# Kernel tuning notes

Measured on AMD Instinct MI355X. Metric: run time of the kernel, lower is better.

The kernel has to match this reference:

```python
import jax, jax.numpy as jnp
import numpy as np

B, S, D, H, HD, F, R = 16, 512, 1024, 16, 64, 4096, 16


def setup_inputs() -> dict:
    key = jax.random.key(0)
    ks = jax.random.split(key, 24)
    sc = 0.02  # keep activations in a sane range through the deep stack
    d = {
        "x": jax.random.normal(ks[0], (B, S, D), jnp.float32),
        "w_q": jax.random.normal(ks[1], (D, D), jnp.float32) * sc,
        "b_q": jnp.zeros((D,), jnp.float32),
        "w_q_lora_a": jax.random.normal(ks[2], (D, R), jnp.float32) * sc,
        "w_q_lora_b": jax.random.normal(ks[3], (R, D), jnp.float32) * sc,
        "w_k": jax.random.normal(ks[4], (D, D), jnp.float32) * sc,
        "b_k": jnp.zeros((D,), jnp.float32),
        "w_k_lora_a": jax.random.normal(ks[5], (D, R), jnp.float32) * sc,
        "w_k_lora_b": jax.random.normal(ks[6], (R, D), jnp.float32) * sc,
        "w_v": jax.random.normal(ks[7], (D, D), jnp.float32) * sc,
        "b_v": jnp.zeros((D,), jnp.float32),
        "w_v_lora_a": jax.random.normal(ks[8], (D, R), jnp.float32) * sc,
        "w_v_lora_b": jax.random.normal(ks[9], (R, D), jnp.float32) * sc,
        "w_o": jax.random.normal(ks[10], (D, D), jnp.float32) * sc,
        "b_o": jnp.zeros((D,), jnp.float32),
        "w_o_lora_a": jax.random.normal(ks[11], (D, R), jnp.float32) * sc,
        "w_o_lora_b": jax.random.normal(ks[12], (R, D), jnp.float32) * sc,
        "norm_weight_1": jnp.ones((D,), jnp.float32),
        "norm_bias_1": jnp.zeros((D,), jnp.float32),
        "w_up": jax.random.normal(ks[13], (D, F), jnp.float32) * sc,
        "b_up": jnp.zeros((F,), jnp.float32),
        "w_up_lora_a": jax.random.normal(ks[14], (D, R), jnp.float32) * sc,
        "w_up_lora_b": jax.random.normal(ks[15], (R, F), jnp.float32) * sc,
        "w_down": jax.random.normal(ks[16], (F, D), jnp.float32) * sc,
        "b_down": jnp.zeros((D,), jnp.float32),
        "w_down_lora_a": jax.random.normal(ks[17], (F, R), jnp.float32) * sc,
        "w_down_lora_b": jax.random.normal(ks[18], (R, D), jnp.float32) * sc,
        "norm_weight_2": jnp.ones((D,), jnp.float32),
        "norm_bias_2": jnp.zeros((D,), jnp.float32),
        "attention_mask": jnp.zeros((B, 1, 1, S), jnp.float32),
        "num_heads": H,
        "head_dim": HD,
    }
    return d


def _lora(x, w, b, a, bb):
    # base (dequantized) matmul + bias + low-rank LoRA path
    return x @ w + b + (x @ a) @ bb


def _layernorm(x, g, b, eps=1e-5):
    mu = jnp.mean(x, axis=-1, keepdims=True)
    var = jnp.mean(jnp.square(x - mu), axis=-1, keepdims=True)
    return (x - mu) * jax.lax.rsqrt(var + eps) * g + b


def reference(x, w_q, b_q, w_q_lora_a, w_q_lora_b, w_k, b_k, w_k_lora_a, w_k_lora_b,
              w_v, b_v, w_v_lora_a, w_v_lora_b, w_o, b_o, w_o_lora_a, w_o_lora_b,
              norm_weight_1, norm_bias_1, w_up, b_up, w_up_lora_a, w_up_lora_b,
              w_down, b_down, w_down_lora_a, w_down_lora_b, norm_weight_2, norm_bias_2,
              attention_mask, num_heads, head_dim):
    b, s, d = x.shape

    def to_heads(t):  # [B,S,D] -> [B,H,S,hd]
        return t.reshape(b, s, num_heads, head_dim).transpose(0, 2, 1, 3)

    q = to_heads(_lora(x, w_q, b_q, w_q_lora_a, w_q_lora_b))
    k = to_heads(_lora(x, w_k, b_k, w_k_lora_a, w_k_lora_b))
    v = to_heads(_lora(x, w_v, b_v, w_v_lora_a, w_v_lora_b))

    scores = jnp.einsum('bhqd,bhkd->bhqk', q, k) / jnp.sqrt(jnp.float32(head_dim))
    scores = scores + attention_mask
    attn = jax.nn.softmax(scores, axis=-1)
    o = jnp.einsum('bhqk,bhkd->bhqd', attn, v)
    o = o.transpose(0, 2, 1, 3).reshape(b, s, d)  # head_to_hidden_shape

    o_final = _lora(o, w_o, b_o, w_o_lora_a, w_o_lora_b) + x
    x_medium = _layernorm(o_final, norm_weight_1, norm_bias_1)

    up = _lora(x_medium, w_up, b_up, w_up_lora_a, w_up_lora_b)
    fn = jax.nn.gelu(up, approximate=False)  # torch F.gelu default (erf)
    down = _lora(fn, w_down, b_down, w_down_lora_a, w_down_lora_b) + x_medium
    x_out = _layernorm(down, norm_weight_2, norm_bias_2)
    return x_out
```

## Files before the change

### kernel.cpp

```cpp
#include <hip/hip_runtime.h>
#include <stdint.h>

typedef __attribute__((ext_vector_type(8))) short bf16x8;
typedef __attribute__((ext_vector_type(4))) float f32x4;
typedef __attribute__((ext_vector_type(8))) unsigned short u16x8;
typedef __attribute__((ext_vector_type(4))) unsigned short u16x4;
typedef __attribute__((address_space(3))) uint32_t as3_u32;
typedef const __attribute__((address_space(1))) uint32_t as1_u32;

#define DEV __device__ __forceinline__

DEV float bf2f(unsigned short u) {
    union { unsigned int i; float f; } x; x.i = ((unsigned int)u) << 16; return x.f;
}
DEV unsigned short f2bf(float f) {
    union { float f; unsigned int i; } x; x.f = f;
    unsigned int i = x.i;
    return (unsigned short)((i + 0x7FFFu + ((i >> 16) & 1u)) >> 16);
}

struct PrepDesc { const float* src; unsigned short* dst; int R, C, ds, gx, base, type; };
struct PrepArgs {
    PrepDesc d[20]; int nd;
    const float* bq; const float* bk; const float* bv; float* bias_out;
};

__global__ __launch_bounds__(256) void k_prep(PrepArgs A) {
    __shared__ float t[32][33];
    int b = blockIdx.x, tid = threadIdx.x;
    int i = 0;
    while (i + 1 < A.nd && A.d[i + 1].base <= b) i++;
    PrepDesc d = A.d[i];
    int local = b - d.base;
    if (d.type == 0) {
        size_t idx = (size_t)local * 256 + tid;
        const float4* p = (const float4*)(d.src + idx * 8);
        float4 a = p[0], c = p[1];
        u16x8 o;
        o[0] = f2bf(a.x); o[1] = f2bf(a.y); o[2] = f2bf(a.z); o[3] = f2bf(a.w);
        o[4] = f2bf(c.x); o[5] = f2bf(c.y); o[6] = f2bf(c.z); o[7] = f2bf(c.w);
        *(u16x8*)(d.dst + idx * 8) = o;
    } else if (d.type == 1) {
        int bx = local % d.gx, by = local / d.gx;
        int c0 = bx * 32, r0 = by * 32;
        int tx = tid & 31, ty = tid >> 5;
#pragma unroll
        for (int k = 0; k < 4; k++) {
            int r = r0 + ty + k * 8, c = c0 + tx;
            t[ty + k * 8][tx] = (r < d.R && c < d.C) ? d.src[(size_t)r * d.C + c] : 0.f;
        }
        __syncthreads();
#pragma unroll
        for (int k = 0; k < 4; k++) {
            int c = c0 + ty + k * 8, r = r0 + tx;
            if (c < d.C && r < d.R) d.dst[(size_t)c * d.ds + r] = f2bf(t[tx][ty + k * 8]);
        }
    } else {
        int idx = local * 256 + tid;
        if (idx < 3072)
            A.bias_out[idx] = (idx < 1024) ? A.bq[idx]
                            : (idx < 2048) ? A.bk[idx - 1024] : A.bv[idx - 2048];
    }
}

struct LoraArgs {
    const unsigned short* in;
    const unsigned short* aT0; const unsigned short* aT1; const unsigned short* aT2;
    unsigned short* out;
    int K, stride, cb0, cb1, cb2;
};
__global__ __launch_bounds__(256) void k_lora(LoraArgs A) {
    int z = blockIdx.y;
    const unsigned short* aT = (z == 0) ? A.aT0 : (z == 1) ? A.aT1 : A.aT2;
    int cb = (z == 0) ? A.cb0 : (z == 1) ? A.cb1 : A.cb2;
    int tid = threadIdx.x, l = tid & 63, w = tid >> 6;
    int lr = l & 15, g = l >> 4;
    int m0 = blockIdx.x * 64 + w * 16;
    const unsigned short* ip = A.in + (size_t)(m0 + lr) * A.K + g * 8;
    const unsigned short* ap = aT + (size_t)lr * A.K + g * 8;
    f32x4 acc = (f32x4){0.f, 0.f, 0.f, 0.f};
    int iters = A.K >> 5;
#pragma unroll 4
    for (int i = 0; i < iters; i++) {
        bf16x8 af = *(const bf16x8*)(ip + i * 32);
        bf16x8 bfr = *(const bf16x8*)(ap + i * 32);
        acc = __builtin_amdgcn_mfma_f32_16x16x32_bf16(af, bfr, acc, 0, 0, 0);
    }
    unsigned short* op = A.out + (size_t)(m0 + g * 4) * A.stride + cb;
#pragma unroll
    for (int r = 0; r < 4; r++) {
        op[(size_t)r * A.stride + lr] = f2bf(acc[r]);
        op[(size_t)r * A.stride + 16 + lr] = 0;
    }
}

struct GemmArgs {
    const unsigned short* A;
    const unsigned short* B;
    const unsigned short* xa;
    const unsigned short* bbT;
    const float* bias;
    const float* res;
    const unsigned short* resb;
    float* outf;
    unsigned short* outb;
    int M, N, K, xa_stride, slice, swz;
};

template <int RES, bool GELU, bool OUTB>
__global__ __launch_bounds__(256, 4) void k_gemm(GemmArgs P) {
    __shared__ __align__(128) unsigned short smem[17408];
    int tid = threadIdx.x, l = tid & 63, w = tid >> 6;
    int wm = w >> 1, wn = w & 1, lr = l & 15, g = l >> 4, h3 = l & 7;

    int n0, m0;
    if (P.swz) {
        int nwg = gridDim.x * gridDim.y;
        int lin = blockIdx.y * gridDim.x + blockIdx.x;
        int wg = (lin & 7) * (nwg >> 3) + (lin >> 3);
        n0 = (wg % gridDim.x) * 128; m0 = (wg / gridDim.x) * 128;
    } else {
        n0 = blockIdx.x * 128; m0 = blockIdx.y * 128;
    }

    const unsigned short* pa[4];
    const unsigned short* pb[4];
#pragma unroll
    for (int i = 0; i < 4; i++) {
        int idx = i * 256 + w * 64 + l;
        int r = idx >> 3, p = idx & 7, cc = p ^ (r & 7);
        pa[i] = P.A + (size_t)(m0 + r) * P.K + cc * 8;
        pb[i] = P.B + (size_t)(n0 + r) * P.K + cc * 8;
    }
    f32x4 acc[4][4];
#pragma unroll
    for (int a = 0; a < 4; a++)
#pragma unroll
        for (int b = 0; b < 4; b++) acc[a][b] = (f32x4){0.f, 0.f, 0.f, 0.f};

    int KT = P.K >> 6;
    for (int kt = 0; kt < KT; kt++) {
#pragma unroll
        for (int i = 0; i < 4; i++) {
            unsigned int base = i * 2048 + w * 512;
            __builtin_amdgcn_global_load_lds((as1_u32*)(pa[i] + kt * 64),
                                             (as3_u32*)(smem + base), 16, 0, 0);
            __builtin_amdgcn_global_load_lds((as1_u32*)(pb[i] + kt * 64),
                                             (as3_u32*)(smem + base + 8192), 16, 0, 0);
        }
        __syncthreads();
        const unsigned short* bufA = smem;
        const unsigned short* bufB = smem + 8192;
#pragma unroll
        for (int ks = 0; ks < 2; ks++) {
            bf16x8 af[4], bfr[4];
#pragma unroll
            for (int mi = 0; mi < 4; mi++) {
                int row = wm * 64 + mi * 16 + lr;
                af[mi] = *(const bf16x8*)(bufA + row * 64 + (((ks * 4 + g) ^ h3) * 8));
            }
#pragma unroll
            for (int ni = 0; ni < 4; ni++) {
                int row = wn * 64 + ni * 16 + lr;
                bfr[ni] = *(const bf16x8*)(bufB + row * 64 + (((ks * 4 + g) ^ h3) * 8));
            }
#pragma unroll
            for (int mi = 0; mi < 4; mi++)
#pragma unroll
                for (int ni = 0; ni < 4; ni++)
                    acc[mi][ni] = __builtin_amdgcn_mfma_f32_16x16x32_bf16(af[mi], bfr[ni],
                                                                          acc[mi][ni], 0, 0, 0);
        }
        __syncthreads();
    }

    int cb = (n0 / P.slice) * 32;
    bf16x8 xf[4], bbf[4];
#pragma unroll
    for (int mi = 0; mi < 4; mi++) {
        int m = m0 + wm * 64 + mi * 16 + lr;
        xf[mi] = *(const bf16x8*)(P.xa + (size_t)m * P.xa_stride + cb + g * 8);
    }
#pragma unroll
    for (int ni = 0; ni < 4; ni++) {
        int n = n0 + wn * 64 + ni * 16 + lr;
        bbf[ni] = *(const bf16x8*)(P.bbT + (size_t)n * 32 + g * 8);
    }
#pragma unroll
    for (int mi = 0; mi < 4; mi++)
#pragma unroll
        for (int ni = 0; ni < 4; ni++)
            acc[mi][ni] = __builtin_amdgcn_mfma_f32_16x16x32_bf16(xf[mi], bbf[ni],
                                                                  acc[mi][ni], 0, 0, 0);

    if constexpr (OUTB) {
        unsigned short* eb = smem;
        const int LS = 136;
#pragma unroll
        for (int ni = 0; ni < 4; ni++) {
            int nn = wn * 64 + ni * 16 + lr;
            float bv = P.bias[n0 + nn];
#pragma unroll
            for (int mi = 0; mi < 4; mi++) {
#pragma unroll
                for (int r = 0; r < 4; r++) {
                    int mm = wm * 64 + mi * 16 + g * 4 + r;
                    float v = acc[mi][ni][r] + bv;
                    if constexpr (RES == 1) v += P.res[(size_t)(m0 + mm) * P.N + n0 + nn];
                    if constexpr (RES == 2) v += bf2f(P.resb[(size_t)(m0 + mm) * P.N + n0 + nn]);
                    if constexpr (GELU) {
                        float u = 0.7978845608f * v * (1.f + 0.044715f * v * v);
                        float e = __expf(2.f * u);
                        v = v - v / (e + 1.f);
                    }
                    eb[mm * LS + nn] = f2bf(v);
                }
            }
        }
        __syncthreads();
#pragma unroll
        for (int i = 0; i < 8; i++) {
            int idx = i * 256 + tid;
            int row = idx >> 4, c = idx & 15;
            u16x8 d = *(const u16x8*)(eb + row * LS + c * 8);
            *(u16x8*)(P.outb + (size_t)(m0 + row) * P.N + n0 + c * 8) = d;
        }
    } else {
#pragma unroll
        for (int ni = 0; ni < 4; ni++) {
            int n = n0 + wn * 64 + ni * 16 + lr;
            float bv = P.bias[n];
#pragma unroll
            for (int mi = 0; mi < 4; mi++) {
#pragma unroll
                for (int r = 0; r < 4; r++) {
                    int m = m0 + wm * 64 + mi * 16 + g * 4 + r;
                    float v = acc[mi][ni][r] + bv;
                    if constexpr (RES == 1) v += P.res[(size_t)m * P.N + n];
                    if constexpr (RES == 2) v += bf2f(P.resb[(size_t)m * P.N + n]);
                    P.outf[(size_t)m * P.N + n] = v;
                }
            }
        }
    }
}

__global__ __launch_bounds__(256) void k_attn(const unsigned short* __restrict__ qkv,
                                              const float* __restrict__ mask,
                                              unsigned short* __restrict__ o) {
    __shared__ __align__(128) unsigned short Kl[64 * 64];
    __shared__ __align__(128) unsigned short Vt[64 * 64];
    __shared__ __align__(128) unsigned short Pl[4 * 16 * 64];
    int tid = threadIdx.x, l = tid & 63, w = tid >> 6;
    int b = blockIdx.y >> 4, h = blockIdx.y & 15;
    int qbase = blockIdx.x * 64;
    int lr = l & 15, g = l >> 4, h3 = l & 7;

    size_t rowQ = (size_t)(b * 512 + qbase + w * 16 + lr) * 3072 + h * 64;
    bf16x8 qf0 = *(const bf16x8*)(qkv + rowQ + g * 8);
    bf16x8 qf1 = *(const bf16x8*)(qkv + rowQ + 32 + g * 8);

    f32x4 oacc[4];
    float mrun[4], lrun[4];
#pragma unroll
    for (int i = 0; i < 4; i++) { oacc[i] = (f32x4){0.f, 0.f, 0.f, 0.f}; mrun[i] = -1e30f; lrun[i] = 0.f; }

    int sr = tid >> 3, sc = tid & 7;
    int cV = tid & 7, kv0 = (tid >> 3) * 2;
    const unsigned short* kbase = qkv + (size_t)(b * 512) * 3072 + 1024 + h * 64;
    const unsigned short* vbase = qkv + (size_t)(b * 512) * 3072 + 2048 + h * 64;
    unsigned short* pw = Pl + w * 1024;

    for (int kt = 0; kt < 8; kt++) {
#pragma unroll
        for (int i = 0; i < 2; i++) {
            int r = sr + i * 32;
            u16x8 kd = *(const u16x8*)(kbase + (size_t)(kt * 64 + r) * 3072 + sc * 8);
            *(u16x8*)(Kl + r * 64 + ((sc ^ (r & 7)) * 8)) = kd;
        }
        {
            u16x8 v0 = *(const u16x8*)(vbase + (size_t)(kt * 64 + kv0) * 3072 + cV * 8);
            u16x8 v1 = *(const u16x8*)(vbase + (size_t)(kt * 64 + kv0 + 1) * 3072 + cV * 8);
            int kc = kv0 >> 3, ke = kv0 & 7;
#pragma unroll
            for (int j = 0; j < 8; j++) {
                int hd = cV * 8 + j;
                unsigned int pr = (unsigned int)v0[j] | ((unsigned int)v1[j] << 16);
                *(unsigned int*)(Vt + hd * 64 + ((kc ^ (hd & 7)) * 8) + ke) = pr;
            }
        }
        __syncthreads();

        f32x4 s[4];
#pragma unroll
        for (int i = 0; i < 4; i++) s[i] = (f32x4){0.f, 0.f, 0.f, 0.f};
#pragma unroll
        for (int ks = 0; ks < 2; ks++) {
            bf16x8 qa = ks ? qf1 : qf0;
#pragma unroll
            for (int nf = 0; nf < 4; nf++) {
                int kr = lr + nf * 16;
                bf16x8 kf = *(const bf16x8*)(Kl + kr * 64 + (((ks * 4 + g) ^ h3) * 8));
                s[nf] = __builtin_amdgcn_mfma_f32_16x16x32_bf16(qa, kf, s[nf], 0, 0, 0);
            }
        }
        const float* mrow = mask + b * 512 + kt * 64;
#pragma unroll
        for (int nf = 0; nf < 4; nf++) {
            float mk = mrow[lr + nf * 16];
            s[nf] = s[nf] * 0.125f + mk;
        }
        float mx[4];
#pragma unroll
        for (int r = 0; r < 4; r++) {
            mx[r] = fmaxf(fmaxf(s[0][r], s[1][r]), fmaxf(s[2][r], s[3][r]));
#pragma unroll
            for (int d = 1; d < 16; d <<= 1) mx[r] = fmaxf(mx[r], __shfl_xor(mx[r], d, 64));
        }
        float al[4];
#pragma unroll
        for (int r = 0; r < 4; r++) {
            float mn = fmaxf(mrun[r], mx[r]);
            al[r] = __expf(mrun[r] - mn);
            mrun[r] = mn;
        }
        float rs[4] = {0.f, 0.f, 0.f, 0.f};
#pragma unroll
        for (int nf = 0; nf < 4; nf++)
#pragma unroll
            for (int r = 0; r < 4; r++) {
                float p = __expf(s[nf][r] - mrun[r]);
                s[nf][r] = p;
                rs[r] += p;
            }
#pragma unroll
        for (int r = 0; r < 4; r++) {
#pragma unroll
            for (int d = 1; d < 16; d <<= 1) rs[r] += __shfl_xor(rs[r], d, 64);
            lrun[r] = lrun[r] * al[r] + rs[r];
        }
#pragma unroll
        for (int nh = 0; nh < 4; nh++) {
            f32x4 t = oacc[nh];
            t[0] *= al[0]; t[1] *= al[1]; t[2] *= al[2]; t[3] *= al[3];
            oacc[nh] = t;
        }
#pragma unroll
        for (int nf = 0; nf < 4; nf++) {
            int pc = lr + nf * 16;
#pragma unroll
            for (int r = 0; r < 4; r++) {
                int prr = g * 4 + r;
                pw[prr * 64 + (((pc >> 3) ^ (prr & 7)) * 8) + (pc & 7)] = f2bf(s[nf][r]);
            }
        }
#pragma unroll
        for (int ks = 0; ks < 2; ks++) {
            bf16x8 pa = *(const bf16x8*)(pw + lr * 64 + (((ks * 4 + g) ^ h3) * 8));
#pragma unroll
            for (int nh = 0; nh < 4; nh++) {
                int vr = lr + nh * 16;
                bf16x8 vf = *(const bf16x8*)(Vt + vr * 64 + (((ks * 4 + g) ^ h3) * 8));
                oacc[nh] = __builtin_amdgcn_mfma_f32_16x16x32_bf16(pa, vf, oacc[nh], 0, 0, 0);
            }
        }
        __syncthreads();
    }
#pragma unroll
    for (int r = 0; r < 4; r++) {
        float inv = 1.f / lrun[r];
        size_t orow = (size_t)(b * 512 + qbase + w * 16 + g * 4 + r) * 1024 + h * 64;
#pragma unroll
        for (int nh = 0; nh < 4; nh++)
            o[orow + lr + nh * 16] = f2bf(oacc[nh][r] * inv);
    }
}

__global__ __launch_bounds__(256) void k_ln_b(const unsigned short* __restrict__ in,
                                              const float* __restrict__ gamma,
                                              const float* __restrict__ beta,
                                              unsigned short* __restrict__ outb) {
    int row = blockIdx.x, tid = threadIdx.x;
    u16x4 raw = *(const u16x4*)(in + (size_t)row * 1024 + tid * 4);
    float v0 = bf2f(raw[0]), v1 = bf2f(raw[1]), v2 = bf2f(raw[2]), v3 = bf2f(raw[3]);
    float s = v0 + v1 + v2 + v3;
    float q = v0 * v0 + v1 * v1 + v2 * v2 + v3 * v3;
#pragma unroll
    for (int d = 1; d < 64; d <<= 1) { s += __shfl_xor(s, d, 64); q += __shfl_xor(q, d, 64); }
    __shared__ float red[8];
    int l = tid & 63, w = tid >> 6;
    if (l == 0) { red[w] = s; red[4 + w] = q; }
    __syncthreads();
    s = red[0] + red[1] + red[2] + red[3];
    q = red[4] + red[5] + red[6] + red[7];
    float mu = s * (1.f / 1024.f);
    float var = q * (1.f / 1024.f) - mu * mu;
    float rstd = rsqrtf(var + 1e-5f);
    float4 g4 = *(const float4*)(gamma + tid * 4);
    float4 b4 = *(const float4*)(beta + tid * 4);
    u16x4 ob;
    ob[0] = f2bf((v0 - mu) * rstd * g4.x + b4.x);
    ob[1] = f2bf((v1 - mu) * rstd * g4.y + b4.y);
    ob[2] = f2bf((v2 - mu) * rstd * g4.z + b4.z);
    ob[3] = f2bf((v3 - mu) * rstd * g4.w + b4.w);
    *(u16x4*)(outb + (size_t)row * 1024 + tid * 4) = ob;
}

__global__ __launch_bounds__(256) void k_ln_bf(const unsigned short* __restrict__ in,
                                               const float* __restrict__ gamma,
                                               const float* __restrict__ beta,
                                               float* __restrict__ outf) {
    int row = blockIdx.x, tid = threadIdx.x;
    u16x4 raw = *(const u16x4*)(in + (size_t)row * 1024 + tid * 4);
    float v0 = bf2f(raw[0]), v1 = bf2f(raw[1]), v2 = bf2f(raw[2]), v3 = bf2f(raw[3]);
    float s = v0 + v1 + v2 + v3;
    float q = v0 * v0 + v1 * v1 + v2 * v2 + v3 * v3;
#pragma unroll
    for (int d = 1; d < 64; d <<= 1) { s += __shfl_xor(s, d, 64); q += __shfl_xor(q, d, 64); }
    __shared__ float red[8];
    int l = tid & 63, w = tid >> 6;
    if (l == 0) { red[w] = s; red[4 + w] = q; }
    __syncthreads();
    s = red[0] + red[1] + red[2] + red[3];
    q = red[4] + red[5] + red[6] + red[7];
    float mu = s * (1.f / 1024.f);
    float var = q * (1.f / 1024.f) - mu * mu;
    float rstd = rsqrtf(var + 1e-5f);
    float4 g4 = *(const float4*)(gamma + tid * 4);
    float4 b4 = *(const float4*)(beta + tid * 4);
    float4 y;
    y.x = (v0 - mu) * rstd * g4.x + b4.x;
    y.y = (v1 - mu) * rstd * g4.y + b4.y;
    y.z = (v2 - mu) * rstd * g4.z + b4.z;
    y.w = (v3 - mu) * rstd * g4.w + b4.w;
    *(float4*)(outf + (size_t)row * 1024 + tid * 4) = y;
}

extern "C" void kernel_launch(void* const* d_in, const int* in_sizes, int n_in,
                              void* d_out, int out_size, void* d_ws, size_t ws_size,
                              hipStream_t stream) {
    const float* x    = (const float*)d_in[0];
    const float* w_q  = (const float*)d_in[1];
    const float* b_q  = (const float*)d_in[2];
    const float* a_q  = (const float*)d_in[3];
    const float* bb_q = (const float*)d_in[4];
    const float* w_k  = (const float*)d_in[5];
    const float* b_k  = (const float*)d_in[6];
    const float* a_k  = (const float*)d_in[7];
    const float* bb_k = (const float*)d_in[8];
    const float* w_v  = (const float*)d_in[9];
    const float* b_v  = (const float*)d_in[10];
    const float* a_v  = (const float*)d_in[11];
    const float* bb_v = (const float*)d_in[12];
    const float* w_o  = (const float*)d_in[13];
    const float* b_o  = (const float*)d_in[14];
    const float* a_o  = (const float*)d_in[15];
    const float* bb_o = (const float*)d_in[16];
    const float* nw1  = (const float*)d_in[17];
    const float* nb1  = (const float*)d_in[18];
    const float* w_up = (const float*)d_in[19];
    const float* b_up = (const float*)d_in[20];
    const float* a_up = (const float*)d_in[21];
    const float* bb_up= (const float*)d_in[22];
    const float* w_dn = (const float*)d_in[23];
    const float* b_dn = (const float*)d_in[24];
    const float* a_dn = (const float*)d_in[25];
    const float* bb_dn= (const float*)d_in[26];
    const float* nw2  = (const float*)d_in[27];
    const float* nb2  = (const float*)d_in[28];
    const float* mask = (const float*)d_in[29];
    float* out = (float*)d_out;

    char* W = (char*)d_ws;
    size_t off = 0;
    auto alloc = [&](size_t bytes) { size_t r = off; off += (bytes + 1023) & ~(size_t)1023; return r; };

    unsigned short* WT_QKV = (unsigned short*)(W + alloc(3072ull * 1024 * 2));
    unsigned short* WT_O   = (unsigned short*)(W + alloc(1024ull * 1024 * 2));
    unsigned short* WT_UP  = (unsigned short*)(W + alloc(4096ull * 1024 * 2));
    unsigned short* WT_DN  = (unsigned short*)(W + alloc(1024ull * 4096 * 2));
    unsigned short* AT_Q   = (unsigned short*)(W + alloc(16ull * 1024 * 2));
    unsigned short* AT_K   = (unsigned short*)(W + alloc(16ull * 1024 * 2));
    unsigned short* AT_V   = (unsigned short*)(W + alloc(16ull * 1024 * 2));
    unsigned short* AT_O   = (unsigned short*)(W + alloc(16ull * 1024 * 2));
    unsigned short* AT_UP  = (unsigned short*)(W + alloc(16ull * 1024 * 2));
    unsigned short* AT_DN  = (unsigned short*)(W + alloc(16ull * 4096 * 2));
    size_t bbt_begin = off;
    unsigned short* BBT_QKV= (unsigned short*)(W + alloc(3072ull * 32 * 2));
    unsigned short* BBT_O  = (unsigned short*)(W + alloc(1024ull * 32 * 2));
    unsigned short* BBT_UP = (unsigned short*)(W + alloc(4096ull * 32 * 2));
    unsigned short* BBT_DN = (unsigned short*)(W + alloc(1024ull * 32 * 2));
    size_t bbt_end = off;
    float* BIAS_QKV        = (float*)(W + alloc(3072ull * 4));
    unsigned short* XA_QKV = (unsigned short*)(W + alloc(8192ull * 96 * 2));
    unsigned short* XA_O   = (unsigned short*)(W + alloc(8192ull * 32 * 2));
    unsigned short* XA_UP  = (unsigned short*)(W + alloc(8192ull * 32 * 2));
    unsigned short* XA_DN  = (unsigned short*)(W + alloc(8192ull * 32 * 2));
    unsigned short* XBF    = (unsigned short*)(W + alloc(8192ull * 1024 * 2));
    unsigned short* BIG    = (unsigned short*)(W + alloc(8192ull * 4096 * 2));
    unsigned short* O_BF   = (unsigned short*)(W + alloc(8192ull * 1024 * 2));
    float* OF              = (float*)(W + alloc(8192ull * 1024 * 4));
    (void)ws_size; (void)in_sizes; (void)n_in; (void)out_size;

    unsigned short* QKV = BIG;
    unsigned short* FN  = BIG;
    unsigned short* XMB = XBF;
    unsigned short* OFB = (unsigned short*)OF;
    unsigned short* DNB = ((unsigned short*)OF) + 8192ull * 1024;

    hipMemsetAsync(W + bbt_begin, 0, bbt_end - bbt_begin, stream);
    {
        PrepArgs pa{};
        int base = 0, i = 0;
        auto add = [&](const float* src, unsigned short* dst, int R, int C, int ds, int type) {
            int cnt;
            if (type == 0) cnt = (R * C) / (256 * 8);
            else if (type == 1) cnt = ((C + 31) / 32) * ((R + 31) / 32);
            else cnt = 12;
            pa.d[i] = {src, dst, R, C, ds, (type == 1) ? (C + 31) / 32 : 1, base, type};
            base += cnt; i++;
        };
        add(x, XBF, 8192, 1024, 0, 0);
        add(w_q, WT_QKV, 1024, 1024, 1024, 1);
        add(w_k, WT_QKV + 1024ull * 1024, 1024, 1024, 1024, 1);
        add(w_v, WT_QKV + 2048ull * 1024, 1024, 1024, 1024, 1);
        add(w_o, WT_O, 1024, 1024, 1024, 1);
        add(w_up, WT_UP, 1024, 4096, 1024, 1);
        add(w_dn, WT_DN, 4096, 1024, 4096, 1);
        add(a_q, AT_Q, 1024, 16, 1024, 1);
        add(a_k, AT_K, 1024, 16, 1024, 1);
        add(a_v, AT_V, 1024, 16, 1024, 1);
        add(a_o, AT_O, 1024, 16, 1024, 1);
        add(a_up, AT_UP, 1024, 16, 1024, 1);
        add(a_dn, AT_DN, 4096, 16, 4096, 1);
        add(bb_q, BBT_QKV, 16, 1024, 32, 1);
        add(bb_k, BBT_QKV + 1024ull * 32, 16, 1024, 32, 1);
        add(bb_v, BBT_QKV + 2048ull * 32, 16, 1024, 32, 1);
        add(bb_o, BBT_O, 16, 1024, 32, 1);
        add(bb_up, BBT_UP, 16, 4096, 32, 1);
        add(bb_dn, BBT_DN, 16, 1024, 32, 1);
        add(nullptr, nullptr, 0, 0, 0, 2);
        pa.nd = i;
        pa.bq = b_q; pa.bk = b_k; pa.bv = b_v; pa.bias_out = BIAS_QKV;
        k_prep<<<dim3(base), dim3(256), 0, stream>>>(pa);
    }
    {
        LoraArgs la{XBF, AT_Q, AT_K, AT_V, XA_QKV, 1024, 96, 0, 32, 64};
        k_lora<<<dim3(128, 3), dim3(256), 0, stream>>>(la);
    }
    {
        GemmArgs ga{XBF, WT_QKV, XA_QKV, BBT_QKV, BIAS_QKV, nullptr, nullptr, nullptr, QKV,
                    8192, 3072, 1024, 96, 1024, 0};
        k_gemm<0, false, true><<<dim3(24, 64), dim3(256), 0, stream>>>(ga);
    }
    k_attn<<<dim3(8, 256), dim3(256), 0, stream>>>(QKV, mask, O_BF);
    {
        LoraArgs la{O_BF, AT_O, AT_O, AT_O, XA_O, 1024, 32, 0, 0, 0};
        k_lora<<<dim3(128, 1), dim3(256), 0, stream>>>(la);
    }
    {
        GemmArgs ga{O_BF, WT_O, XA_O, BBT_O, b_o, x, nullptr, nullptr, OFB,
                    8192, 1024, 1024, 32, 1024, 1};
        k_gemm<1, false, true><<<dim3(8, 64), dim3(256), 0, stream>>>(ga);
    }
    k_ln_b<<<dim3(8192), dim3(256), 0, stream>>>(OFB, nw1, nb1, XMB);
    {
        LoraArgs la{XMB, AT_UP, AT_UP, AT_UP, XA_UP, 1024, 32, 0, 0, 0};
        k_lora<<<dim3(128, 1), dim3(256), 0, stream>>>(la);
    }
    {
        GemmArgs ga{XMB, WT_UP, XA_UP, BBT_UP, b_up, nullptr, nullptr, nullptr, FN,
                    8192, 4096, 1024, 32, 4096, 0};
        k_gemm<0, true, true><<<dim3(32, 64), dim3(256), 0, stream>>>(ga);
    }
    {
        LoraArgs la{FN, AT_DN, AT_DN, AT_DN, XA_DN, 4096, 32, 0, 0, 0};
        k_lora<<<dim3(128, 1), dim3(256), 0, stream>>>(la);
    }
    {
        GemmArgs ga{FN, WT_DN, XA_DN, BBT_DN, b_dn, nullptr, XMB, nullptr, DNB,
                    8192, 1024, 4096, 32, 1024, 1};
        k_gemm<2, false, true><<<dim3(8, 64), dim3(256), 0, stream>>>(ga);
    }
    k_ln_bf<<<dim3(8192), dim3(256), 0, stream>>>(DNB, nw2, nb2, out);
}
```

Baseline: 454.7 us.

## Fold LoRA low-rank update into dense weights during prep, drop LoRA kernels

```diff
diff --git a/kernel.cpp b/kernel.cpp
--- a/kernel.cpp
+++ b/kernel.cpp
@@ -19,14 +19,19 @@
     return (unsigned short)((i + 0x7FFFu + ((i >> 16) & 1u)) >> 16);
 }
 
-struct PrepDesc { const float* src; unsigned short* dst; int R, C, ds, gx, base, type; };
+struct PrepDesc {
+    const float* src; const float* a; const float* bb; unsigned short* dst;
+    int R, C, ds, gx, base, type;
+};
 struct PrepArgs {
-    PrepDesc d[20]; int nd;
+    PrepDesc d[10]; int nd;
     const float* bq; const float* bk; const float* bv; float* bias_out;
 };
 
 __global__ __launch_bounds__(256) void k_prep(PrepArgs A) {
     __shared__ float t[32][33];
+    __shared__ float aL[32][17];
+    __shared__ float bbL[16][33];
     int b = blockIdx.x, tid = threadIdx.x;
     int i = 0;
     while (i + 1 < A.nd && A.d[i + 1].base <= b) i++;
@@ -40,7 +45,7 @@
         o[0] = f2bf(a.x); o[1] = f2bf(a.y); o[2] = f2bf(a.z); o[3] = f2bf(a.w);
         o[4] = f2bf(c.x); o[5] = f2bf(c.y); o[6] = f2bf(c.z); o[7] = f2bf(c.w);
         *(u16x8*)(d.dst + idx * 8) = o;
-    } else if (d.type == 1) {
+    } else if (d.type == 3) {
         int bx = local % d.gx, by = local / d.gx;
         int c0 = bx * 32, r0 = by * 32;
         int tx = tid & 31, ty = tid >> 5;
@@ -49,11 +54,32 @@
             int r = r0 + ty + k * 8, c = c0 + tx;
             t[ty + k * 8][tx] = (r < d.R && c < d.C) ? d.src[(size_t)r * d.C + c] : 0.f;
         }
+        {
+            int idx = tid * 2;
+            int i0 = idx >> 4, j0 = idx & 15;
+            aL[i0][j0] = (r0 + i0 < d.R) ? d.a[(size_t)(r0 + i0) * 16 + j0] : 0.f;
+            int idx1 = idx + 1;
+            int i1 = idx1 >> 4, j1 = idx1 & 15;
+            aL[i1][j1] = (r0 + i1 < d.R) ? d.a[(size_t)(r0 + i1) * 16 + j1] : 0.f;
+        }
+        {
+            int idx = tid * 2;
+            int j0 = idx >> 5, i0 = idx & 31;
+            bbL[j0][i0] = (c0 + i0 < d.C) ? d.bb[(size_t)j0 * d.C + c0 + i0] : 0.f;
+            int idx1 = idx + 1;
+            int j1 = idx1 >> 5, i1 = idx1 & 31;
+            bbL[j1][i1] = (c0 + i1 < d.C) ? d.bb[(size_t)j1 * d.C + c0 + i1] : 0.f;
+        }
         __syncthreads();
 #pragma unroll
         for (int k = 0; k < 4; k++) {
             int c = c0 + ty + k * 8, r = r0 + tx;
-            if (c < d.C && r < d.R) d.dst[(size_t)c * d.ds + r] = f2bf(t[tx][ty + k * 8]);
+            if (c < d.C && r < d.R) {
+                float acc = t[tx][ty + k * 8];
+#pragma unroll
+                for (int j = 0; j < 16; j++) acc += aL[tx][j] * bbL[j][ty + k * 8];
+                d.dst[(size_t)c * d.ds + r] = f2bf(acc);
+            }
         }
     } else {
         int idx = local * 256 + tid;
@@ -63,48 +89,15 @@
     }
 }
 
-struct LoraArgs {
-    const unsigned short* in;
-    const unsigned short* aT0; const unsigned short* aT1; const unsigned short* aT2;
-    unsigned short* out;
-    int K, stride, cb0, cb1, cb2;
-};
-__global__ __launch_bounds__(256) void k_lora(LoraArgs A) {
-    int z = blockIdx.y;
-    const unsigned short* aT = (z == 0) ? A.aT0 : (z == 1) ? A.aT1 : A.aT2;
-    int cb = (z == 0) ? A.cb0 : (z == 1) ? A.cb1 : A.cb2;
-    int tid = threadIdx.x, l = tid & 63, w = tid >> 6;
-    int lr = l & 15, g = l >> 4;
-    int m0 = blockIdx.x * 64 + w * 16;
-    const unsigned short* ip = A.in + (size_t)(m0 + lr) * A.K + g * 8;
-    const unsigned short* ap = aT + (size_t)lr * A.K + g * 8;
-    f32x4 acc = (f32x4){0.f, 0.f, 0.f, 0.f};
-    int iters = A.K >> 5;
-#pragma unroll 4
-    for (int i = 0; i < iters; i++) {
-        bf16x8 af = *(const bf16x8*)(ip + i * 32);
-        bf16x8 bfr = *(const bf16x8*)(ap + i * 32);
-        acc = __builtin_amdgcn_mfma_f32_16x16x32_bf16(af, bfr, acc, 0, 0, 0);
-    }
-    unsigned short* op = A.out + (size_t)(m0 + g * 4) * A.stride + cb;
-#pragma unroll
-    for (int r = 0; r < 4; r++) {
-        op[(size_t)r * A.stride + lr] = f2bf(acc[r]);
-        op[(size_t)r * A.stride + 16 + lr] = 0;
-    }
-}
-
 struct GemmArgs {
     const unsigned short* A;
     const unsigned short* B;
-    const unsigned short* xa;
-    const unsigned short* bbT;
     const float* bias;
     const float* res;
     const unsigned short* resb;
     float* outf;
     unsigned short* outb;
-    int M, N, K, xa_stride, slice, swz;
+    int M, N, K, swz;
 };
 
 template <int RES, bool GELU, bool OUTB>
@@ -173,25 +166,6 @@
         }
         __syncthreads();
     }
-
-    int cb = (n0 / P.slice) * 32;
-    bf16x8 xf[4], bbf[4];
-#pragma unroll
-    for (int mi = 0; mi < 4; mi++) {
-        int m = m0 + wm * 64 + mi * 16 + lr;
-        xf[mi] = *(const bf16x8*)(P.xa + (size_t)m * P.xa_stride + cb + g * 8);
-    }
-#pragma unroll
-    for (int ni = 0; ni < 4; ni++) {
-        int n = n0 + wn * 64 + ni * 16 + lr;
-        bbf[ni] = *(const bf16x8*)(P.bbT + (size_t)n * 32 + g * 8);
-    }
-#pragma unroll
-    for (int mi = 0; mi < 4; mi++)
-#pragma unroll
-        for (int ni = 0; ni < 4; ni++)
-            acc[mi][ni] = __builtin_amdgcn_mfma_f32_16x16x32_bf16(xf[mi], bbf[ni],
-                                                                  acc[mi][ni], 0, 0, 0);
 
     if constexpr (OUTB) {
         unsigned short* eb = smem;
@@ -479,107 +453,62 @@
     unsigned short* WT_O   = (unsigned short*)(W + alloc(1024ull * 1024 * 2));
     unsigned short* WT_UP  = (unsigned short*)(W + alloc(4096ull * 1024 * 2));
     unsigned short* WT_DN  = (unsigned short*)(W + alloc(1024ull * 4096 * 2));
-    unsigned short* AT_Q   = (unsigned short*)(W + alloc(16ull * 1024 * 2));
-    unsigned short* AT_K   = (unsigned short*)(W + alloc(16ull * 1024 * 2));
-    unsigned short* AT_V   = (unsigned short*)(W + alloc(16ull * 1024 * 2));
-    unsigned short* AT_O   = (unsigned short*)(W + alloc(16ull * 1024 * 2));
-    unsigned short* AT_UP  = (unsigned short*)(W + alloc(16ull * 1024 * 2));
-    unsigned short* AT_DN  = (unsigned short*)(W + alloc(16ull * 4096 * 2));
-    size_t bbt_begin = off;
-    unsigned short* BBT_QKV= (unsigned short*)(W + alloc(3072ull * 32 * 2));
-    unsigned short* BBT_O  = (unsigned short*)(W + alloc(1024ull * 32 * 2));
-    unsigned short* BBT_UP = (unsigned short*)(W + alloc(4096ull * 32 * 2));
-    unsigned short* BBT_DN = (unsigned short*)(W + alloc(1024ull * 32 * 2));
-    size_t bbt_end = off;
     float* BIAS_QKV        = (float*)(W + alloc(3072ull * 4));
-    unsigned short* XA_QKV = (unsigned short*)(W + alloc(8192ull * 96 * 2));
-    unsigned short* XA_O   = (unsigned short*)(W + alloc(8192ull * 32 * 2));
-    unsigned short* XA_UP  = (unsigned short*)(W + alloc(8192ull * 32 * 2));
-    unsigned short* XA_DN  = (unsigned short*)(W + alloc(8192ull * 32 * 2));
     unsigned short* XBF    = (unsigned short*)(W + alloc(8192ull * 1024 * 2));
     unsigned short* BIG    = (unsigned short*)(W + alloc(8192ull * 4096 * 2));
     unsigned short* O_BF   = (unsigned short*)(W + alloc(8192ull * 1024 * 2));
-    float* OF              = (float*)(W + alloc(8192ull * 1024 * 4));
+    unsigned short* OFB    = (unsigned short*)(W + alloc(8192ull * 1024 * 2));
+    unsigned short* DNB    = (unsigned short*)(W + alloc(8192ull * 1024 * 2));
     (void)ws_size; (void)in_sizes; (void)n_in; (void)out_size;
 
     unsigned short* QKV = BIG;
     unsigned short* FN  = BIG;
     unsigned short* XMB = XBF;
-    unsigned short* OFB = (unsigned short*)OF;
-    unsigned short* DNB = ((unsigned short*)OF) + 8192ull * 1024;
-
-    hipMemsetAsync(W + bbt_begin, 0, bbt_end - bbt_begin, stream);
+
     {
         PrepArgs pa{};
         int base = 0, i = 0;
-        auto add = [&](const float* src, unsigned short* dst, int R, int C, int ds, int type) {
+        auto add = [&](const float* src, const float* a, const float* bb,
+                       unsigned short* dst, int R, int C, int ds, int type) {
             int cnt;
             if (type == 0) cnt = (R * C) / (256 * 8);
-            else if (type == 1) cnt = ((C + 31) / 32) * ((R + 31) / 32);
+            else if (type == 3) cnt = ((C + 31) / 32) * ((R + 31) / 32);
             else cnt = 12;
-            pa.d[i] = {src, dst, R, C, ds, (type == 1) ? (C + 31) / 32 : 1, base, type};
+            pa.d[i] = {src, a, bb, dst, R, C, ds, (type == 3) ? (C + 31) / 32 : 1, base, type};
             base += cnt; i++;
         };
-        add(x, XBF, 8192, 1024, 0, 0);
-        add(w_q, WT_QKV, 1024, 1024, 1024, 1);
-        add(w_k, WT_QKV + 1024ull * 1024, 1024, 1024, 1024, 1);
-        add(w_v, WT_QKV + 2048ull * 1024, 1024, 1024, 1024, 1);
-        add(w_o, WT_O, 1024, 1024, 1024, 1);
-        add(w_up, WT_UP, 1024, 4096, 1024, 1);
-        add(w_dn, WT_DN, 4096, 1024, 4096, 1);
-        add(a_q, AT_Q, 1024, 16, 1024, 1);
-        add(a_k, AT_K, 1024, 16, 1024, 1);
-        add(a_v, AT_V, 1024, 16, 1024, 1);
-        add(a_o, AT_O, 1024, 16, 1024, 1);
-        add(a_up, AT_UP, 1024, 16, 1024, 1);
-        add(a_dn, AT_DN, 4096, 16, 4096, 1);
-        add(bb_q, BBT_QKV, 16, 1024, 32, 1);
-        add(bb_k, BBT_QKV + 1024ull * 32, 16, 1024, 32, 1);
-        add(bb_v, BBT_QKV + 2048ull * 32, 16, 1024, 32, 1);
-        add(bb_o, BBT_O, 16, 1024, 32, 1);
-        add(bb_up, BBT_UP, 16, 4096, 32, 1);
-        add(bb_dn, BBT_DN, 16, 1024, 32, 1);
-        add(nullptr, nullptr, 0, 0, 0, 2);
+        add(x, nullptr, nullptr, XBF, 8192, 1024, 0, 0);
+        add(w_q, a_q, bb_q, WT_QKV, 1024, 1024, 1024, 3);
+        add(w_k, a_k, bb_k, WT_QKV + 1024ull * 1024, 1024, 1024, 1024, 3);
+        add(w_v, a_v, bb_v, WT_QKV + 2048ull * 1024, 1024, 1024, 1024, 3);
+        add(w_o, a_o, bb_o, WT_O, 1024, 1024, 1024, 3);
+        add(w_up, a_up, bb_up, WT_UP, 1024, 4096, 1024, 3);
+        add(w_dn, a_dn, bb_dn, WT_DN, 4096, 1024, 4096, 3);
+        add(nullptr, nullptr, nullptr, nullptr, 0, 0, 0, 2);
         pa.nd = i;
         pa.bq = b_q; pa.bk = b_k; pa.bv = b_v; pa.bias_out = BIAS_QKV;
         k_prep<<<dim3(base), dim3(256), 0, stream>>>(pa);
     }
     {
-        LoraArgs la{XBF, AT_Q, AT_K, AT_V, XA_QKV, 1024, 96, 0, 32, 64};
-        k_lora<<<dim3(128, 3), dim3(256), 0, stream>>>(la);
-    }
-    {
-        GemmArgs ga{XBF, WT_QKV, XA_QKV, BBT_QKV, BIAS_QKV, nullptr, nullptr, nullptr, QKV,
-                    8192, 3072, 1024, 96, 1024, 0};
+        GemmArgs ga{XBF, WT_QKV, BIAS_QKV, nullptr, nullptr, nullptr, QKV,
+                    8192, 3072, 1024, 0};
         k_gemm<0, false, true><<<dim3(24, 64), dim3(256), 0, stream>>>(ga);
     }
     k_attn<<<dim3(8, 256), dim3(256), 0, stream>>>(QKV, mask, O_BF);
     {
-        LoraArgs la{O_BF, AT_O, AT_O, AT_O, XA_O, 1024, 32, 0, 0, 0};
-        k_lora<<<dim3(128, 1), dim3(256), 0, stream>>>(la);
-    }
-    {
-        GemmArgs ga{O_BF, WT_O, XA_O, BBT_O, b_o, x, nullptr, nullptr, OFB,
-                    8192, 1024, 1024, 32, 1024, 1};
+        GemmArgs ga{O_BF, WT_O, b_o, x, nullptr, nullptr, OFB,
+                    8192, 1024, 1024, 1};
         k_gemm<1, false, true><<<dim3(8, 64), dim3(256), 0, stream>>>(ga);
     }
     k_ln_b<<<dim3(8192), dim3(256), 0, stream>>>(OFB, nw1, nb1, XMB);
     {
-        LoraArgs la{XMB, AT_UP, AT_UP, AT_UP, XA_UP, 1024, 32, 0, 0, 0};
-        k_lora<<<dim3(128, 1), dim3(256), 0, stream>>>(la);
+        GemmArgs ga{XMB, WT_UP, b_up, nullptr, nullptr, nullptr, FN,
+                    8192, 4096, 1024, 0};
+        k_gemm<0, true, true><<<dim3(32, 64), dim3(256), 0, stream>>>(ga);
     }
     {
-        GemmArgs ga{XMB, WT_UP, XA_UP, BBT_UP, b_up, nullptr, nullptr, nullptr, FN,
-                    8192, 4096, 1024, 32, 4096, 0};
-        k_gemm<0, true, true><<<dim3(32, 64), dim3(256), 0, stream>>>(ga);
-    }
-    {
-        LoraArgs la{FN, AT_DN, AT_DN, AT_DN, XA_DN, 4096, 32, 0, 0, 0};
-        k_lora<<<dim3(128, 1), dim3(256), 0, stream>>>(la);
-    }
-    {
-        GemmArgs ga{FN, WT_DN, XA_DN, BBT_DN, b_dn, nullptr, XMB, nullptr, DNB,
-                    8192, 1024, 4096, 32, 1024, 1};
+        GemmArgs ga{FN, WT_DN, b_dn, nullptr, XMB, nullptr, DNB,
+                    8192, 1024, 4096, 1};
         k_gemm<2, false, true><<<dim3(8, 64), dim3(256), 0, stream>>>(ga);
     }
     k_ln_bf<<<dim3(8192), dim3(256), 0, stream>>>(DNB, nw2, nb2, out);
```

New measurement: 385.3 us, median of 2. -15.3%, faster.
